# Performance work log

Hardware: AMD Instinct MI355X
Metric: run time of the kernel (lower is better)

Reference implementation:

```python
import jax, jax.numpy as jnp
import numpy as np

B, J, D, W, H, EH, L = 128, 8192, 32, 4, 128, 256, 32
TEMP = 1.0


def _ln(x, g, b, eps=1e-5):
    mu = jnp.mean(x, axis=-1, keepdims=True)
    var = jnp.var(x, axis=-1, keepdims=True)
    return (x - mu) * jax.lax.rsqrt(var + eps) * g + b


def setup_inputs() -> dict:
    key = jax.random.key(0)
    ks = jax.random.split(key, 12)

    def lin(k, fi, fo):
        k1, k2 = jax.random.split(k)
        s = 1.0 / np.sqrt(fi)
        return (jax.random.uniform(k1, (fi, fo), minval=-s, maxval=s, dtype=jnp.float32),
                jax.random.uniform(k2, (fo,), minval=-s, maxval=s, dtype=jnp.float32))

    h_w1, h_b1 = lin(ks[0], 1 + D, H)
    h_w2, h_b2 = lin(ks[1], H, D)
    g_w1, g_b1 = lin(ks[2], D, D // 2)
    g_w2, g_b2 = lin(ks[3], D // 2, W)
    c_w, c_b = lin(ks[4], W * D, D)
    e_w1, e_b1 = lin(ks[5], D, EH)
    e_w2, e_b2 = lin(ks[6], EH, 2 * L)
    return {
        'x': jax.random.normal(ks[7], (B, J), dtype=jnp.float32),
        'mask': jax.random.randint(ks[8], (B, J), 0, 2, dtype=jnp.int32),
        'fe': jax.random.normal(ks[9], (J, D), dtype=jnp.float32),
        'h_w1': h_w1, 'h_b1': h_b1,
        'h_ln1_w': jnp.ones((H,), jnp.float32), 'h_ln1_b': jnp.zeros((H,), jnp.float32),
        'h_w2': h_w2, 'h_b2': h_b2,
        'h_ln2_w': jnp.ones((D,), jnp.float32), 'h_ln2_b': jnp.zeros((D,), jnp.float32),
        'g_w1': g_w1, 'g_b1': g_b1, 'g_w2': g_w2, 'g_b2': g_b2,
        'c_w': c_w, 'c_b': c_b,
        'c_ln_w': jnp.ones((D,), jnp.float32), 'c_ln_b': jnp.zeros((D,), jnp.float32),
        'e_w1': e_w1, 'e_b1': e_b1,
        'e_ln1_w': jnp.ones((EH,), jnp.float32), 'e_ln1_b': jnp.zeros((EH,), jnp.float32),
        'e_w2': e_w2, 'e_b2': e_b2,
        'e_ln2_w': jnp.ones((2 * L,), jnp.float32), 'e_ln2_b': jnp.zeros((2 * L,), jnp.float32),
    }


def _forward(x, mask, fe, h_w1, h_b1, h_ln1_w, h_ln1_b, h_w2, h_b2, h_ln2_w, h_ln2_b,
             g_w1, g_b1, g_w2, g_b2, c_w, c_b, c_ln_w, c_ln_b,
             e_w1, e_b1, e_ln1_w, e_ln1_b, e_w2, e_b2, e_ln2_w, e_ln2_b):
    relu = jax.nn.relu
    # h_in = concat([x, F]) @ h_w1 split into scalar column + shared embedding part
    # (fe @ h_w1[1:]) is [J,H], shared across cells -> avoids materializing [B,J,1+D]
    pre = x[..., None] * h_w1[0][None, None, :] + (fe @ h_w1[1:])[None] + h_b1  # [B,J,H]
    h1 = relu(_ln(pre, h_ln1_w, h_ln1_b))
    h_out = relu(_ln(h1 @ h_w2 + h_b2, h_ln2_w, h_ln2_b))  # [B,J,D]
    raw_gates = relu(h_out @ g_w1 + g_b1) @ g_w2 + g_b2  # [B,J,W]
    logits = jnp.clip(raw_gates * TEMP, -10.0, 10.0)
    logits = jnp.where(mask[..., None] > 0, logits, -1e9)  # masked gather -> -inf fill
    weights = jax.nn.softmax(logits, axis=1)  # softmax over observed junctions
    head_sums = jnp.einsum('bjw,bjd->bwd', weights, h_out)  # [B,W,D]
    comb = relu(_ln(head_sums.reshape(head_sums.shape[0], -1) @ c_w + c_b, c_ln_w, c_ln_b))
    comb = jnp.where((jnp.sum(mask, axis=1) > 0)[:, None], comb, 0.0)  # zero cells -> zeros
    h = relu(_ln(comb @ e_w1 + e_b1, e_ln1_w, e_ln1_b))
    o = relu(_ln(h @ e_w2 + e_b2, e_ln2_w, e_ln2_b))
    mu, logvar = jnp.split(o, 2, axis=-1)
    return mu, logvar


def reference(x, mask, fe, h_w1, h_b1, h_ln1_w, h_ln1_b, h_w2, h_b2, h_ln2_w, h_ln2_b,
              g_w1, g_b1, g_w2, g_b2, c_w, c_b, c_ln_w, c_ln_b,
              e_w1, e_b1, e_ln1_w, e_ln1_b, e_w2, e_b2, e_ln2_w, e_ln2_b):
    return _forward(x, mask, fe, h_w1, h_b1, h_ln1_w, h_ln1_b, h_w2, h_b2, h_ln2_w, h_ln2_b,
                    g_w1, g_b1, g_w2, g_b2, c_w, c_b, c_ln_w, c_ln_b,
                    e_w1, e_b1, e_ln1_w, e_ln1_b, e_w2, e_b2, e_ln2_w, e_ln2_b)
```

## Files before the change

### kernel.cpp

```cpp
#include <hip/hip_runtime.h>
#include <cstdint>

#define BDIM 128
#define JDIM 8192

typedef short s8x __attribute__((ext_vector_type(8)));
typedef float f4x __attribute__((ext_vector_type(4)));
typedef float f2x __attribute__((ext_vector_type(2)));

__device__ __forceinline__ unsigned short bf16u(float f) {
    return __builtin_bit_cast(unsigned short, (__bf16)f);
}
__device__ __forceinline__ unsigned int pkbf(float lo, float hi) {
    return (unsigned int)bf16u(lo) | ((unsigned int)bf16u(hi) << 16);
}
__device__ __forceinline__ f2x upk(unsigned int w) {
    f2x r;
    r.x = __uint_as_float(w << 16);
    r.y = __uint_as_float(w & 0xffff0000u);
    return r;
}
__device__ __forceinline__ f2x pkfma(f2x a, f2x b, f2x c) {
#if __has_builtin(__builtin_elementwise_fma)
    return __builtin_elementwise_fma(a, b, c);
#else
    f2x r; r.x = fmaf(a.x, b.x, c.x); r.y = fmaf(a.y, b.y, c.y); return r;
#endif
}
__device__ __forceinline__ f2x pkmax0(f2x a) {
#if __has_builtin(__builtin_elementwise_max)
    f2x z = {0.f, 0.f};
    return __builtin_elementwise_max(a, z);
#else
    f2x r; r.x = fmaxf(a.x, 0.f); r.y = fmaxf(a.y, 0.f); return r;
#endif
}

template <int CTRL>
__device__ __forceinline__ float dppadd(float x) {
    int y = __builtin_amdgcn_update_dpp(0, __builtin_bit_cast(int, x), CTRL, 0xF, 0xF, true);
    return x + __builtin_bit_cast(float, y);
}
__device__ __forceinline__ float allred16(float x) {
    x = dppadd<0xB1>(x);
    x = dppadd<0x4E>(x);
    x = dppadd<0x141>(x);
    x = dppadd<0x140>(x);
    return x;
}

__global__ __launch_bounds__(128) void k_prep(
    const float* __restrict__ fe, const float* __restrict__ hw1,
    const float* __restrict__ hb1,
    const float* __restrict__ hw2, const float* __restrict__ gw1,
    unsigned short* __restrict__ feWb, float* __restrict__ aux,
    float* __restrict__ scal, uint4* __restrict__ fragW)
{
    const int j = blockIdx.x, h = threadIdx.x;
    float acc = hb1[h];
#pragma unroll
    for (int d = 0; d < 32; ++d)
        acc = fmaf(fe[j * 32 + d], hw1[(1 + d) * 128 + h], acc);
    feWb[(size_t)j * 128 + h] = bf16u(acc);

    const float w0h = hw1[h];
    float s1 = acc, sx = w0h * acc, s2 = acc * acc;
#pragma unroll
    for (int m = 1; m <= 32; m <<= 1) {
        s1 += __shfl_xor(s1, m); sx += __shfl_xor(sx, m); s2 += __shfl_xor(s2, m);
    }
    __shared__ float red[2][3];
    const int wv = threadIdx.x >> 6, ln = threadIdx.x & 63;
    if (ln == 0) { red[wv][0] = s1; red[wv][1] = sx; red[wv][2] = s2; }
    __syncthreads();
    if (threadIdx.x == 0) {
        aux[j * 4 + 0] = (red[0][0] + red[1][0]) * (1.f / 128.f);
        aux[j * 4 + 1] = (red[0][1] + red[1][1]) * (1.f / 128.f);
        aux[j * 4 + 2] = (red[0][2] + red[1][2]) * (1.f / 128.f);
    }
    if (j == 0) {
        float a = w0h, b = w0h * w0h;
#pragma unroll
        for (int m = 1; m <= 32; m <<= 1) { a += __shfl_xor(a, m); b += __shfl_xor(b, m); }
        __syncthreads();
        if (ln == 0) { red[wv][0] = a; red[wv][1] = b; }
        __syncthreads();
        if (threadIdx.x == 0) {
            scal[0] = (red[0][0] + red[1][0]) * (1.f / 128.f);
            scal[1] = (red[0][1] + red[1][1]) * (1.f / 128.f);
        }
        if (threadIdx.x < 64) {
            const int cc = threadIdx.x & 15, gg = threadIdx.x >> 4;
#pragma unroll
            for (int nt = 0; nt < 2; ++nt)
#pragma unroll
                for (int t = 0; t < 4; ++t) {
                    const int kb = 32 * t + 8 * gg, n = 16 * nt + cc;
                    uint4 u;
                    u.x = pkbf(hw2[(kb + 0) * 32 + n], hw2[(kb + 1) * 32 + n]);
                    u.y = pkbf(hw2[(kb + 2) * 32 + n], hw2[(kb + 3) * 32 + n]);
                    u.z = pkbf(hw2[(kb + 4) * 32 + n], hw2[(kb + 5) * 32 + n]);
                    u.w = pkbf(hw2[(kb + 6) * 32 + n], hw2[(kb + 7) * 32 + n]);
                    fragW[(nt * 4 + t) * 64 + threadIdx.x] = u;
                }
            uint4 u;
            u.x = pkbf(gw1[(8 * gg + 0) * 16 + cc], gw1[(8 * gg + 1) * 16 + cc]);
            u.y = pkbf(gw1[(8 * gg + 2) * 16 + cc], gw1[(8 * gg + 3) * 16 + cc]);
            u.z = pkbf(gw1[(8 * gg + 4) * 16 + cc], gw1[(8 * gg + 5) * 16 + cc]);
            u.w = pkbf(gw1[(8 * gg + 6) * 16 + cc], gw1[(8 * gg + 7) * 16 + cc]);
            fragW[8 * 64 + threadIdx.x] = u;
        }
    }
}

__global__ __launch_bounds__(256, 2) void k_main(
    const float* __restrict__ x, const int* __restrict__ mask,
    const unsigned short* __restrict__ feWb, const float* __restrict__ aux,
    const float* __restrict__ scal, const uint4* __restrict__ fragW,
    const float* __restrict__ hw1, const float* __restrict__ ln1w,
    const float* __restrict__ ln1b,
    const float* __restrict__ hb2,
    const float* __restrict__ ln2w, const float* __restrict__ ln2b,
    const float* __restrict__ gb1,
    const float* __restrict__ gw2, const float* __restrict__ gb2,
    float* __restrict__ P, float* __restrict__ SEb, int njb, int jpw)
{
    __shared__ float w0s[128], g1s[128], b1s[128];
    __shared__ float holds[8][576];
    __shared__ float hsL[2048];
    __shared__ float seL[64];

    const int tid = threadIdx.x, l = tid & 63;
    const int wv = __builtin_amdgcn_readfirstlane(tid >> 6);
    const int c = l & 15, g = l >> 4;
    const int bt = blockIdx.y, bx = blockIdx.x;
    const int b0 = bt * 16;

    if (tid < 128) { w0s[tid] = hw1[tid]; g1s[tid] = ln1w[tid]; b1s[tid] = ln1b[tid]; }
    __syncthreads();

    const float mw0 = scal[0], q0 = scal[1];

    s8x wf[2][4];
#pragma unroll
    for (int nt = 0; nt < 2; ++nt)
#pragma unroll
        for (int t = 0; t < 4; ++t)
            wf[nt][t] = __builtin_bit_cast(s8x, fragW[(nt * 4 + t) * 64 + l]);
    const s8x g1f = __builtin_bit_cast(s8x, fragW[8 * 64 + l]);

    const float hb2a = hb2[c],      hb2b = hb2[16 + c];
    const float g2a  = ln2w[c],     g2b  = ln2w[16 + c];
    const float z2a  = ln2b[c],     z2b  = ln2b[16 + c];
    const float gb1c = gb1[c];
    float gw2c[4], gb2v[4];
#pragma unroll
    for (int w = 0; w < 4; ++w) { gw2c[w] = gw2[c * 4 + w]; gb2v[w] = gb2[w]; }

    const int j0 = (bx * 4 + wv) * jpw;
    const float* xrow = x + (size_t)(b0 + c) * JDIM;
    const int*   mrow = mask + (size_t)(b0 + c) * JDIM;

    f2x   hsacc[4][4];
    float seacc[4][4];
#pragma unroll
    for (int r = 0; r < 4; ++r)
#pragma unroll
        for (int w = 0; w < 4; ++w) {
            hsacc[r][w].x = 0.f; hsacc[r][w].y = 0.f; seacc[r][w] = 0.f;
        }

    for (int jj = 0; jj < jpw; ++jj) {
        const int j = j0 + jj;
        const float xv = xrow[j];
        const int   mv = mrow[j];
        const float4 au = *(const float4*)(aux + j * 4);
        const float m1 = au.x, qx = au.y, q2 = au.z;
        const float mu = fmaf(xv, mw0, m1);
        const float e2 = fmaf(xv * xv, q0, fmaf(2.f * xv, qx, q2));
        const float rs = rsqrtf(e2 - mu * mu + 1e-5f);
        const float nms = -mu * rs;
        const f2x xv2 = {xv, xv}, rs2 = {rs, rs}, nm2 = {nms, nms};

        f4x ca = {0.f, 0.f, 0.f, 0.f}, cbv = {0.f, 0.f, 0.f, 0.f};
        const unsigned short* fj = feWb + (size_t)j * 128;
#pragma unroll
        for (int t = 0; t < 4; ++t) {
            const int kb = 32 * t + 8 * g;
            const uint4 fw = *(const uint4*)(fj + kb);
            const unsigned int fwv[4] = {fw.x, fw.y, fw.z, fw.w};
            const f2x* wp = (const f2x*)&w0s[kb];
            const f2x* gp = (const f2x*)&g1s[kb];
            const f2x* bp = (const f2x*)&b1s[kb];
            unsigned int res[4];
#pragma unroll
            for (int p = 0; p < 4; ++p) {
                f2x h2 = pkfma(xv2, wp[p], upk(fwv[p]));
                h2 = pkfma(h2, rs2, nm2);
                h2 = pkfma(h2, gp[p], bp[p]);
                h2 = pkmax0(h2);
                res[p] = pkbf(h2.x, h2.y);
            }
            const uint4 u = make_uint4(res[0], res[1], res[2], res[3]);
            const s8x af = __builtin_bit_cast(s8x, u);
            ca  = __builtin_amdgcn_mfma_f32_16x16x32_bf16(af, wf[0][t], ca,  0, 0, 0);
            cbv = __builtin_amdgcn_mfma_f32_16x16x32_bf16(af, wf[1][t], cbv, 0, 0, 0);
        }

        float v0[4], v1[4], sr[4], qr[4];
#pragma unroll
        for (int r = 0; r < 4; ++r) {
            v0[r] = ca[r] + hb2a;
            v1[r] = cbv[r] + hb2b;
            sr[r] = v0[r] + v1[r];
            qr[r] = v0[r] * v0[r] + v1[r] * v1[r];
        }
#pragma unroll
        for (int r = 0; r < 4; ++r) { sr[r] = allred16(sr[r]); qr[r] = allred16(qr[r]); }
        float ho0[4], ho1[4];
#pragma unroll
        for (int r = 0; r < 4; ++r) {
            const float m2  = sr[r] * 0.03125f;
            const float rs2b = rsqrtf(fmaf(qr[r], 0.03125f, -m2 * m2) + 1e-5f);
            const float nm2b = -m2 * rs2b;
            ho0[r] = fmaxf(fmaf(fmaf(v0[r], rs2b, nm2b), g2a, z2a), 0.f);
            ho1[r] = fmaxf(fmaf(fmaf(v1[r], rs2b, nm2b), g2b, z2b), 0.f);
        }

        float* hp = &holds[wv * 2 + (jj & 1)][0];
#pragma unroll
        for (int r = 0; r < 4; ++r) {
            hp[(4 * g + r) * 36 + c]      = ho0[r];
            hp[(4 * g + r) * 36 + 16 + c] = ho1[r];
        }
        asm volatile("s_waitcnt lgkmcnt(0)" ::: "memory");
        const float4 ra  = *(const float4*)&hp[c * 36 + 8 * g];
        const float4 rb2 = *(const float4*)&hp[c * 36 + 8 * g + 4];
        uint4 ua;
        ua.x = pkbf(ra.x, ra.y);  ua.y = pkbf(ra.z, ra.w);
        ua.z = pkbf(rb2.x, rb2.y); ua.w = pkbf(rb2.z, rb2.w);
        const s8x af2 = __builtin_bit_cast(s8x, ua);
        f4x gc = {0.f, 0.f, 0.f, 0.f};
        gc = __builtin_amdgcn_mfma_f32_16x16x32_bf16(af2, g1f, gc, 0, 0, 0);

        float pw[16];
#pragma unroll
        for (int r = 0; r < 4; ++r) {
            const float g1r = fmaxf(gc[r] + gb1c, 0.f);
#pragma unroll
            for (int w = 0; w < 4; ++w) pw[r * 4 + w] = g1r * gw2c[w];
        }
#pragma unroll
        for (int i = 0; i < 16; ++i) pw[i] = allred16(pw[i]);

        const unsigned bm = (unsigned)__ballot(mv > 0);
        float fm[4];
#pragma unroll
        for (int r = 0; r < 4; ++r) fm[r] = (float)((bm >> (4 * g + r)) & 1u);

#pragma unroll
        for (int r = 0; r < 4; ++r) {
            const f2x ho2 = {ho0[r], ho1[r]};
#pragma unroll
            for (int w = 0; w < 4; ++w) {
                const float lg = __builtin_amdgcn_fmed3f(pw[r * 4 + w] + gb2v[w], -10.f, 10.f);
                const float e  = fm[r] * __builtin_amdgcn_exp2f(
                                     fmaf(lg, 1.44269504089f, -14.4269504089f));
                seacc[r][w] += e;
                const f2x e2v = {e, e};
                hsacc[r][w] = pkfma(e2v, ho2, hsacc[r][w]);
            }
        }
    }

    for (int ww = 0; ww < 4; ++ww) {
        __syncthreads();
        if (wv == ww) {
#pragma unroll
            for (int r = 0; r < 4; ++r)
#pragma unroll
                for (int w = 0; w < 4; ++w)
#pragma unroll
                    for (int nt = 0; nt < 2; ++nt) {
                        const int idx = ((4 * g + r) * 4 + w) * 32 + c + 16 * nt;
                        const float val = nt ? hsacc[r][w].y : hsacc[r][w].x;
                        if (ww == 0) hsL[idx] = val;
                        else         hsL[idx] += val;
                    }
            if (c == 0) {
#pragma unroll
                for (int r = 0; r < 4; ++r)
#pragma unroll
                    for (int w = 0; w < 4; ++w) {
                        const int si = (4 * g + r) * 4 + w;
                        if (ww == 0) seL[si] = seacc[r][w];
                        else         seL[si] += seacc[r][w];
                    }
            }
        }
    }
    __syncthreads();
    const size_t base = ((size_t)bt * njb + bx) * 2048;
    for (int i = tid; i < 2048; i += 256) P[base + i] = hsL[i];
    if (tid < 64) SEb[((size_t)bt * njb + bx) * 64 + tid] = seL[tid];
}

__global__ __launch_bounds__(128) void k_tail(
    const float* __restrict__ P, const float* __restrict__ SEb,
    const float* __restrict__ cw, const float* __restrict__ cbv,
    const float* __restrict__ clnw, const float* __restrict__ clnb,
    const float* __restrict__ ew1, const float* __restrict__ eb1,
    const float* __restrict__ l1w, const float* __restrict__ l1b,
    const float* __restrict__ ew2, const float* __restrict__ eb2,
    const float* __restrict__ l2w, const float* __restrict__ l2b,
    float* __restrict__ out, int njb)
{
    const int b = blockIdx.x, t = threadIdx.x;
    const int bt = b >> 4, bi = b & 15;
    __shared__ float hsLs[128], combL[32], hL[256], seW[4], sred[64], red[4];

    const float* Pb = P + (size_t)bt * njb * 2048 + bi * 128;
    float sacc = 0.f;
#pragma unroll 4
    for (int jc = 0; jc < njb; ++jc) sacc += Pb[(size_t)jc * 2048 + t];

    if (t < 64) {
        const int w = t & 3, part = t >> 2;
        float sp = 0.f;
        for (int q = part; q < njb; q += 16)
            sp += SEb[((size_t)bt * njb + q) * 64 + bi * 4 + w];
        sred[t] = sp;
    }
    __syncthreads();
    if (t < 4) {
        float v = 0.f;
#pragma unroll
        for (int sl = 0; sl < 16; ++sl) v += sred[sl * 4 + t];
        seW[t] = v;
    }
    __syncthreads();
    const bool has = seW[0] > 0.f;
    hsLs[t] = has ? sacc / seW[t >> 5] : 0.f;
    __syncthreads();

    if (t < 32) {
        float cv = cbv[t];
#pragma unroll 4
        for (int f = 0; f < 128; ++f) cv = fmaf(hsLs[f], cw[f * 32 + t], cv);
        float s = cv, q = cv * cv;
#pragma unroll
        for (int m = 1; m <= 16; m <<= 1) { s += __shfl_xor(s, m); q += __shfl_xor(q, m); }
        const float mu = s * (1.f / 32.f);
        const float rsg = rsqrtf(fmaf(q, 1.f / 32.f, -mu * mu) + 1e-5f);
        const float v = fmaf(fmaf(cv, rsg, -mu * rsg), clnw[t], clnb[t]);
        combL[t] = has ? fmaxf(v, 0.f) : 0.f;
    }
    __syncthreads();

    float h0 = eb1[t], h1v = eb1[t + 128];
#pragma unroll 4
    for (int d = 0; d < 32; ++d) {
        const float cd = combL[d];
        h0  = fmaf(cd, ew1[d * 256 + t], h0);
        h1v = fmaf(cd, ew1[d * 256 + t + 128], h1v);
    }
    {
        float s = h0 + h1v, q = h0 * h0 + h1v * h1v;
#pragma unroll
        for (int m = 1; m <= 32; m <<= 1) { s += __shfl_xor(s, m); q += __shfl_xor(q, m); }
        const int wv = t >> 6, ln = t & 63;
        if (ln == 0) { red[wv * 2] = s; red[wv * 2 + 1] = q; }
    }
    __syncthreads();
    {
        const float S = red[0] + red[2], Q = red[1] + red[3];
        const float mu1 = S * (1.f / 256.f);
        const float rs1 = rsqrtf(fmaf(Q, 1.f / 256.f, -mu1 * mu1) + 1e-5f);
        hL[t]       = fmaxf(fmaf(fmaf(h0,  rs1, -mu1 * rs1), l1w[t],       l1b[t]),       0.f);
        hL[t + 128] = fmaxf(fmaf(fmaf(h1v, rs1, -mu1 * rs1), l1w[t + 128], l1b[t + 128]), 0.f);
    }
    __syncthreads();

    if (t < 64) {
        float ov = eb2[t];
#pragma unroll 4
        for (int m = 0; m < 256; ++m) ov = fmaf(hL[m], ew2[m * 64 + t], ov);
        float s = ov, q = ov * ov;
#pragma unroll
        for (int m = 1; m <= 32; m <<= 1) { s += __shfl_xor(s, m); q += __shfl_xor(q, m); }
        const float mu2 = s * (1.f / 64.f);
        const float rs2 = rsqrtf(fmaf(q, 1.f / 64.f, -mu2 * mu2) + 1e-5f);
        const float o = fmaxf(fmaf(fmaf(ov, rs2, -mu2 * rs2), l2w[t], l2b[t]), 0.f);
        if (t < 32) out[b * 32 + t] = o;
        else        out[4096 + b * 32 + (t - 32)] = o;
    }
}

extern "C" void kernel_launch(void* const* d_in, const int* in_sizes, int n_in,
                              void* d_out, int out_size, void* d_ws, size_t ws_size,
                              hipStream_t stream)
{
    (void)in_sizes; (void)n_in; (void)out_size;
    const float* x    = (const float*)d_in[0];
    const int*   mask = (const int*)d_in[1];
    const float* fe   = (const float*)d_in[2];
    const float* hw1  = (const float*)d_in[3];
    const float* hb1  = (const float*)d_in[4];
    const float* ln1w = (const float*)d_in[5];
    const float* ln1b = (const float*)d_in[6];
    const float* hw2  = (const float*)d_in[7];
    const float* hb2  = (const float*)d_in[8];
    const float* ln2w = (const float*)d_in[9];
    const float* ln2b = (const float*)d_in[10];
    const float* gw1  = (const float*)d_in[11];
    const float* gb1  = (const float*)d_in[12];
    const float* gw2  = (const float*)d_in[13];
    const float* gb2  = (const float*)d_in[14];
    const float* cw   = (const float*)d_in[15];
    const float* cbv  = (const float*)d_in[16];
    const float* clnw = (const float*)d_in[17];
    const float* clnb = (const float*)d_in[18];
    const float* ew1  = (const float*)d_in[19];
    const float* eb1  = (const float*)d_in[20];
    const float* l1w  = (const float*)d_in[21];
    const float* l1b  = (const float*)d_in[22];
    const float* ew2  = (const float*)d_in[23];
    const float* eb2  = (const float*)d_in[24];
    const float* l2w  = (const float*)d_in[25];
    const float* l2b  = (const float*)d_in[26];

    const size_t fragOff = (2u << 20) + (128u << 10) + 256u;
    const size_t base    = fragOff + 9u * 64u * 16u;
    int NJB = 128;
    {
        const size_t need = base + (size_t)8 * 128 * 2048 * 4 + (size_t)8 * 128 * 64 * 4;
        if (ws_size < need) NJB = 64;
    }
    const int JPW = JDIM / (NJB * 4);

    char* ws = (char*)d_ws;
    unsigned short* feWb = (unsigned short*)ws;
    float* aux   = (float*)(ws + (2u << 20));
    float* scal  = (float*)(ws + (2u << 20) + (128u << 10));
    uint4* fragW = (uint4*)(ws + fragOff);
    float* P     = (float*)(ws + base);
    float* SEb   = (float*)(ws + base + (size_t)8 * NJB * 2048 * 4);

    hipLaunchKernelGGL(k_prep, dim3(JDIM), dim3(128), 0, stream,
                       fe, hw1, hb1, hw2, gw1, feWb, aux, scal, fragW);
    hipLaunchKernelGGL(k_main, dim3(NJB, 8), dim3(256), 0, stream,
                       x, mask, feWb, aux, scal, fragW,
                       hw1, ln1w, ln1b, hb2, ln2w, ln2b,
                       gb1, gw2, gb2, P, SEb, NJB, JPW);
    hipLaunchKernelGGL(k_tail, dim3(BDIM), dim3(128), 0, stream,
                       P, SEb, cw, cbv, clnw, clnb,
                       ew1, eb1, l1w, l1b, ew2, eb2, l2w, l2b,
                       (float*)d_out, NJB);
}
```

Measured before the change: 247.4 us.

## Process junction pairs per iteration, template JPW, batch prep rows, fuse DPP adds

The main loop now handles two junctions per iteration, so the MFMA chains, LDS round-trips and DPP reductions of two independent rows can interleave. JPW becomes a template parameter so the loop bound is known at compile time. The prep kernel processes eight junctions per block and keeps the hw1 column in registers, replacing 8192 tiny blocks with 1024. The all-reduce now uses inline-asm DPP-fused v_add, and the clamp/exp2 constants are folded into a single fma plus med3. Register pressure rises with the doubled live state, which may limit occupancy under the launch bound of two blocks per SIMD.

```diff
diff --git a/kernel.cpp b/kernel.cpp
--- a/kernel.cpp
+++ b/kernel.cpp
@@ -21,31 +21,23 @@
     return r;
 }
 __device__ __forceinline__ f2x pkfma(f2x a, f2x b, f2x c) {
-#if __has_builtin(__builtin_elementwise_fma)
     return __builtin_elementwise_fma(a, b, c);
-#else
-    f2x r; r.x = fmaf(a.x, b.x, c.x); r.y = fmaf(a.y, b.y, c.y); return r;
-#endif
 }
 __device__ __forceinline__ f2x pkmax0(f2x a) {
-#if __has_builtin(__builtin_elementwise_max)
     f2x z = {0.f, 0.f};
     return __builtin_elementwise_max(a, z);
-#else
-    f2x r; r.x = fmaxf(a.x, 0.f); r.y = fmaxf(a.y, 0.f); return r;
-#endif
-}
-
-template <int CTRL>
-__device__ __forceinline__ float dppadd(float x) {
-    int y = __builtin_amdgcn_update_dpp(0, __builtin_bit_cast(int, x), CTRL, 0xF, 0xF, true);
-    return x + __builtin_bit_cast(float, y);
-}
+}
+
 __device__ __forceinline__ float allred16(float x) {
-    x = dppadd<0xB1>(x);
-    x = dppadd<0x4E>(x);
-    x = dppadd<0x141>(x);
-    x = dppadd<0x140>(x);
+    float t;
+    asm("v_add_f32 %0, %1, %1 quad_perm:[1,0,3,2] row_mask:0xf bank_mask:0xf"
+        : "=v"(t) : "v"(x));
+    asm("v_add_f32 %0, %1, %1 quad_perm:[2,3,0,1] row_mask:0xf bank_mask:0xf"
+        : "=v"(x) : "v"(t));
+    asm("v_add_f32 %0, %1, %1 row_half_mirror row_mask:0xf bank_mask:0xf"
+        : "=v"(t) : "v"(x));
+    asm("v_add_f32 %0, %1, %1 row_mirror row_mask:0xf bank_mask:0xf"
+        : "=v"(x) : "v"(t));
     return x;
 }
 
@@ -56,41 +48,50 @@
     unsigned short* __restrict__ feWb, float* __restrict__ aux,
     float* __restrict__ scal, uint4* __restrict__ fragW)
 {
-    const int j = blockIdx.x, h = threadIdx.x;
-    float acc = hb1[h];
-#pragma unroll
-    for (int d = 0; d < 32; ++d)
-        acc = fmaf(fe[j * 32 + d], hw1[(1 + d) * 128 + h], acc);
-    feWb[(size_t)j * 128 + h] = bf16u(acc);
-
+    const int h = threadIdx.x;
+    __shared__ float red[2][3];
+    const int wv = h >> 6, ln = h & 63;
+    float w1r[32];
+#pragma unroll
+    for (int d = 0; d < 32; ++d) w1r[d] = hw1[(1 + d) * 128 + h];
+    const float hb = hb1[h];
     const float w0h = hw1[h];
-    float s1 = acc, sx = w0h * acc, s2 = acc * acc;
-#pragma unroll
-    for (int m = 1; m <= 32; m <<= 1) {
-        s1 += __shfl_xor(s1, m); sx += __shfl_xor(sx, m); s2 += __shfl_xor(s2, m);
-    }
-    __shared__ float red[2][3];
-    const int wv = threadIdx.x >> 6, ln = threadIdx.x & 63;
-    if (ln == 0) { red[wv][0] = s1; red[wv][1] = sx; red[wv][2] = s2; }
-    __syncthreads();
-    if (threadIdx.x == 0) {
-        aux[j * 4 + 0] = (red[0][0] + red[1][0]) * (1.f / 128.f);
-        aux[j * 4 + 1] = (red[0][1] + red[1][1]) * (1.f / 128.f);
-        aux[j * 4 + 2] = (red[0][2] + red[1][2]) * (1.f / 128.f);
-    }
-    if (j == 0) {
+
+    for (int q = 0; q < 8; ++q) {
+        const int j = blockIdx.x * 8 + q;
+        float acc = hb;
+#pragma unroll
+        for (int d = 0; d < 32; ++d) acc = fmaf(fe[j * 32 + d], w1r[d], acc);
+        feWb[(size_t)j * 128 + h] = bf16u(acc);
+
+        float s1 = acc, sx = w0h * acc, s2 = acc * acc;
+#pragma unroll
+        for (int m = 1; m <= 32; m <<= 1) {
+            s1 += __shfl_xor(s1, m); sx += __shfl_xor(sx, m); s2 += __shfl_xor(s2, m);
+        }
+        if (q) __syncthreads();
+        if (ln == 0) { red[wv][0] = s1; red[wv][1] = sx; red[wv][2] = s2; }
+        __syncthreads();
+        if (h == 0) {
+            aux[j * 4 + 0] = (red[0][0] + red[1][0]) * (1.f / 128.f);
+            aux[j * 4 + 1] = (red[0][1] + red[1][1]) * (1.f / 128.f);
+            aux[j * 4 + 2] = (red[0][2] + red[1][2]) * (1.f / 128.f);
+        }
+    }
+
+    if (blockIdx.x == 0) {
         float a = w0h, b = w0h * w0h;
 #pragma unroll
         for (int m = 1; m <= 32; m <<= 1) { a += __shfl_xor(a, m); b += __shfl_xor(b, m); }
         __syncthreads();
         if (ln == 0) { red[wv][0] = a; red[wv][1] = b; }
         __syncthreads();
-        if (threadIdx.x == 0) {
+        if (h == 0) {
             scal[0] = (red[0][0] + red[1][0]) * (1.f / 128.f);
             scal[1] = (red[0][1] + red[1][1]) * (1.f / 128.f);
         }
-        if (threadIdx.x < 64) {
-            const int cc = threadIdx.x & 15, gg = threadIdx.x >> 4;
+        if (h < 64) {
+            const int cc = h & 15, gg = h >> 4;
 #pragma unroll
             for (int nt = 0; nt < 2; ++nt)
 #pragma unroll
@@ -101,18 +102,19 @@
                     u.y = pkbf(hw2[(kb + 2) * 32 + n], hw2[(kb + 3) * 32 + n]);
                     u.z = pkbf(hw2[(kb + 4) * 32 + n], hw2[(kb + 5) * 32 + n]);
                     u.w = pkbf(hw2[(kb + 6) * 32 + n], hw2[(kb + 7) * 32 + n]);
-                    fragW[(nt * 4 + t) * 64 + threadIdx.x] = u;
+                    fragW[(nt * 4 + t) * 64 + h] = u;
                 }
             uint4 u;
             u.x = pkbf(gw1[(8 * gg + 0) * 16 + cc], gw1[(8 * gg + 1) * 16 + cc]);
             u.y = pkbf(gw1[(8 * gg + 2) * 16 + cc], gw1[(8 * gg + 3) * 16 + cc]);
             u.z = pkbf(gw1[(8 * gg + 4) * 16 + cc], gw1[(8 * gg + 5) * 16 + cc]);
             u.w = pkbf(gw1[(8 * gg + 6) * 16 + cc], gw1[(8 * gg + 7) * 16 + cc]);
-            fragW[8 * 64 + threadIdx.x] = u;
-        }
-    }
-}
-
+            fragW[8 * 64 + h] = u;
+        }
+    }
+}
+
+template <int JPW>
 __global__ __launch_bounds__(256, 2) void k_main(
     const float* __restrict__ x, const int* __restrict__ mask,
     const unsigned short* __restrict__ feWb, const float* __restrict__ aux,
@@ -123,7 +125,7 @@
     const float* __restrict__ ln2w, const float* __restrict__ ln2b,
     const float* __restrict__ gb1,
     const float* __restrict__ gw2, const float* __restrict__ gb2,
-    float* __restrict__ P, float* __restrict__ SEb, int njb, int jpw)
+    float* __restrict__ P, float* __restrict__ SEb, int njb)
 {
     __shared__ float w0s[128], g1s[128], b1s[128];
     __shared__ float holds[8][576];
@@ -153,11 +155,15 @@
     const float g2a  = ln2w[c],     g2b  = ln2w[16 + c];
     const float z2a  = ln2b[c],     z2b  = ln2b[16 + c];
     const float gb1c = gb1[c];
-    float gw2c[4], gb2v[4];
-#pragma unroll
-    for (int w = 0; w < 4; ++w) { gw2c[w] = gw2[c * 4 + w]; gb2v[w] = gb2[w]; }
-
-    const int j0 = (bx * 4 + wv) * jpw;
+    const float L2E  = 1.442695040888963f;
+    float gw2c[4], gb2l[4];
+#pragma unroll
+    for (int w = 0; w < 4; ++w) {
+        gw2c[w] = gw2[c * 4 + w];
+        gb2l[w] = fmaf(gb2[w], L2E, -10.f * L2E);
+    }
+
+    const int j0 = (bx * 4 + wv) * JPW;
     const float* xrow = x + (size_t)(b0 + c) * JDIM;
     const int*   mrow = mask + (size_t)(b0 + c) * JDIM;
 
@@ -170,105 +176,128 @@
             hsacc[r][w].x = 0.f; hsacc[r][w].y = 0.f; seacc[r][w] = 0.f;
         }
 
-    for (int jj = 0; jj < jpw; ++jj) {
-        const int j = j0 + jj;
-        const float xv = xrow[j];
-        const int   mv = mrow[j];
-        const float4 au = *(const float4*)(aux + j * 4);
-        const float m1 = au.x, qx = au.y, q2 = au.z;
-        const float mu = fmaf(xv, mw0, m1);
-        const float e2 = fmaf(xv * xv, q0, fmaf(2.f * xv, qx, q2));
-        const float rs = rsqrtf(e2 - mu * mu + 1e-5f);
-        const float nms = -mu * rs;
-        const f2x xv2 = {xv, xv}, rs2 = {rs, rs}, nm2 = {nms, nms};
-
-        f4x ca = {0.f, 0.f, 0.f, 0.f}, cbv = {0.f, 0.f, 0.f, 0.f};
-        const unsigned short* fj = feWb + (size_t)j * 128;
-#pragma unroll
-        for (int t = 0; t < 4; ++t) {
-            const int kb = 32 * t + 8 * g;
-            const uint4 fw = *(const uint4*)(fj + kb);
-            const unsigned int fwv[4] = {fw.x, fw.y, fw.z, fw.w};
-            const f2x* wp = (const f2x*)&w0s[kb];
-            const f2x* gp = (const f2x*)&g1s[kb];
-            const f2x* bp = (const f2x*)&b1s[kb];
-            unsigned int res[4];
-#pragma unroll
-            for (int p = 0; p < 4; ++p) {
-                f2x h2 = pkfma(xv2, wp[p], upk(fwv[p]));
-                h2 = pkfma(h2, rs2, nm2);
-                h2 = pkfma(h2, gp[p], bp[p]);
-                h2 = pkmax0(h2);
-                res[p] = pkbf(h2.x, h2.y);
-            }
-            const uint4 u = make_uint4(res[0], res[1], res[2], res[3]);
-            const s8x af = __builtin_bit_cast(s8x, u);
-            ca  = __builtin_amdgcn_mfma_f32_16x16x32_bf16(af, wf[0][t], ca,  0, 0, 0);
-            cbv = __builtin_amdgcn_mfma_f32_16x16x32_bf16(af, wf[1][t], cbv, 0, 0, 0);
-        }
-
-        float v0[4], v1[4], sr[4], qr[4];
-#pragma unroll
-        for (int r = 0; r < 4; ++r) {
-            v0[r] = ca[r] + hb2a;
-            v1[r] = cbv[r] + hb2b;
-            sr[r] = v0[r] + v1[r];
-            qr[r] = v0[r] * v0[r] + v1[r] * v1[r];
-        }
-#pragma unroll
-        for (int r = 0; r < 4; ++r) { sr[r] = allred16(sr[r]); qr[r] = allred16(qr[r]); }
-        float ho0[4], ho1[4];
-#pragma unroll
-        for (int r = 0; r < 4; ++r) {
-            const float m2  = sr[r] * 0.03125f;
-            const float rs2b = rsqrtf(fmaf(qr[r], 0.03125f, -m2 * m2) + 1e-5f);
-            const float nm2b = -m2 * rs2b;
-            ho0[r] = fmaxf(fmaf(fmaf(v0[r], rs2b, nm2b), g2a, z2a), 0.f);
-            ho1[r] = fmaxf(fmaf(fmaf(v1[r], rs2b, nm2b), g2b, z2b), 0.f);
-        }
-
-        float* hp = &holds[wv * 2 + (jj & 1)][0];
-#pragma unroll
-        for (int r = 0; r < 4; ++r) {
-            hp[(4 * g + r) * 36 + c]      = ho0[r];
-            hp[(4 * g + r) * 36 + 16 + c] = ho1[r];
+    for (int jp = 0; jp < JPW / 2; ++jp) {
+        const int jb = j0 + jp * 2;
+
+        float xv[2], rsv[2], nms[2]; int mv[2];
+#pragma unroll
+        for (int p = 0; p < 2; ++p) {
+            xv[p] = xrow[jb + p];
+            mv[p] = mrow[jb + p];
+            const float4 au = *(const float4*)(aux + (size_t)(jb + p) * 4);
+            const float mu = fmaf(xv[p], mw0, au.x);
+            const float e2 = fmaf(xv[p] * xv[p], q0, fmaf(2.f * xv[p], au.y, au.z));
+            rsv[p] = rsqrtf(e2 - mu * mu + 1e-5f);
+            nms[p] = -mu * rsv[p];
+        }
+
+        f4x ca[2], cb[2];
+#pragma unroll
+        for (int p = 0; p < 2; ++p) { ca[p] = f4x{0.f,0.f,0.f,0.f}; cb[p] = f4x{0.f,0.f,0.f,0.f}; }
+#pragma unroll
+        for (int p = 0; p < 2; ++p) {
+            const f2x xv2 = {xv[p], xv[p]}, rs2 = {rsv[p], rsv[p]}, nm2 = {nms[p], nms[p]};
+            const unsigned short* fj = feWb + (size_t)(jb + p) * 128;
+#pragma unroll
+            for (int t = 0; t < 4; ++t) {
+                const int kb = 32 * t + 8 * g;
+                const uint4 fw = *(const uint4*)(fj + kb);
+                const unsigned int fwv[4] = {fw.x, fw.y, fw.z, fw.w};
+                const f2x* wp = (const f2x*)&w0s[kb];
+                const f2x* gp = (const f2x*)&g1s[kb];
+                const f2x* bp = (const f2x*)&b1s[kb];
+                unsigned int res[4];
+#pragma unroll
+                for (int q = 0; q < 4; ++q) {
+                    f2x h2 = pkfma(xv2, wp[q], upk(fwv[q]));
+                    h2 = pkfma(h2, rs2, nm2);
+                    h2 = pkfma(h2, gp[q], bp[q]);
+                    h2 = pkmax0(h2);
+                    res[q] = pkbf(h2.x, h2.y);
+                }
+                const uint4 u = make_uint4(res[0], res[1], res[2], res[3]);
+                const s8x af = __builtin_bit_cast(s8x, u);
+                ca[p] = __builtin_amdgcn_mfma_f32_16x16x32_bf16(af, wf[0][t], ca[p], 0, 0, 0);
+                cb[p] = __builtin_amdgcn_mfma_f32_16x16x32_bf16(af, wf[1][t], cb[p], 0, 0, 0);
+            }
+        }
+
+        float ho0[2][4], ho1[2][4];
+#pragma unroll
+        for (int p = 0; p < 2; ++p) {
+            float v0[4], v1[4], sr[4], qr[4];
+#pragma unroll
+            for (int r = 0; r < 4; ++r) {
+                v0[r] = ca[p][r] + hb2a;
+                v1[r] = cb[p][r] + hb2b;
+                sr[r] = v0[r] + v1[r];
+                qr[r] = v0[r] * v0[r] + v1[r] * v1[r];
+            }
+#pragma unroll
+            for (int r = 0; r < 4; ++r) { sr[r] = allred16(sr[r]); qr[r] = allred16(qr[r]); }
+#pragma unroll
+            for (int r = 0; r < 4; ++r) {
+                const float m2   = sr[r] * 0.03125f;
+                const float rs2b = rsqrtf(fmaf(qr[r], 0.03125f, -m2 * m2) + 1e-5f);
+                const float nm2b = -m2 * rs2b;
+                ho0[p][r] = fmaxf(fmaf(fmaf(v0[r], rs2b, nm2b), g2a, z2a), 0.f);
+                ho1[p][r] = fmaxf(fmaf(fmaf(v1[r], rs2b, nm2b), g2b, z2b), 0.f);
+            }
+        }
+
+#pragma unroll
+        for (int p = 0; p < 2; ++p) {
+            float* hp = &holds[wv * 2 + p][0];
+#pragma unroll
+            for (int r = 0; r < 4; ++r) {
+                hp[(4 * g + r) * 36 + c]      = ho0[p][r];
+                hp[(4 * g + r) * 36 + 16 + c] = ho1[p][r];
+            }
         }
         asm volatile("s_waitcnt lgkmcnt(0)" ::: "memory");
-        const float4 ra  = *(const float4*)&hp[c * 36 + 8 * g];
-        const float4 rb2 = *(const float4*)&hp[c * 36 + 8 * g + 4];
-        uint4 ua;
-        ua.x = pkbf(ra.x, ra.y);  ua.y = pkbf(ra.z, ra.w);
-        ua.z = pkbf(rb2.x, rb2.y); ua.w = pkbf(rb2.z, rb2.w);
-        const s8x af2 = __builtin_bit_cast(s8x, ua);
-        f4x gc = {0.f, 0.f, 0.f, 0.f};
-        gc = __builtin_amdgcn_mfma_f32_16x16x32_bf16(af2, g1f, gc, 0, 0, 0);
-
-        float pw[16];
-#pragma unroll
-        for (int r = 0; r < 4; ++r) {
-            const float g1r = fmaxf(gc[r] + gb1c, 0.f);
-#pragma unroll
-            for (int w = 0; w < 4; ++w) pw[r * 4 + w] = g1r * gw2c[w];
-        }
-#pragma unroll
-        for (int i = 0; i < 16; ++i) pw[i] = allred16(pw[i]);
-
-        const unsigned bm = (unsigned)__ballot(mv > 0);
-        float fm[4];
-#pragma unroll
-        for (int r = 0; r < 4; ++r) fm[r] = (float)((bm >> (4 * g + r)) & 1u);
-
-#pragma unroll
-        for (int r = 0; r < 4; ++r) {
-            const f2x ho2 = {ho0[r], ho1[r]};
-#pragma unroll
-            for (int w = 0; w < 4; ++w) {
-                const float lg = __builtin_amdgcn_fmed3f(pw[r * 4 + w] + gb2v[w], -10.f, 10.f);
-                const float e  = fm[r] * __builtin_amdgcn_exp2f(
-                                     fmaf(lg, 1.44269504089f, -14.4269504089f));
-                seacc[r][w] += e;
-                const f2x e2v = {e, e};
-                hsacc[r][w] = pkfma(e2v, ho2, hsacc[r][w]);
+        f4x gc[2];
+#pragma unroll
+        for (int p = 0; p < 2; ++p) {
+            const float* hp = &holds[wv * 2 + p][0];
+            const float4 ra  = *(const float4*)&hp[c * 36 + 8 * g];
+            const float4 rb2 = *(const float4*)&hp[c * 36 + 8 * g + 4];
+            uint4 ua;
+            ua.x = pkbf(ra.x, ra.y);   ua.y = pkbf(ra.z, ra.w);
+            ua.z = pkbf(rb2.x, rb2.y); ua.w = pkbf(rb2.z, rb2.w);
+            const s8x af2 = __builtin_bit_cast(s8x, ua);
+            f4x z = {0.f, 0.f, 0.f, 0.f};
+            gc[p] = __builtin_amdgcn_mfma_f32_16x16x32_bf16(af2, g1f, z, 0, 0, 0);
+        }
+
+#pragma unroll
+        for (int p = 0; p < 2; ++p) {
+            float pw[16];
+#pragma unroll
+            for (int r = 0; r < 4; ++r) {
+                const float g1r = fmaxf(gc[p][r] + gb1c, 0.f);
+#pragma unroll
+                for (int w = 0; w < 4; ++w) pw[r * 4 + w] = g1r * gw2c[w];
+            }
+#pragma unroll
+            for (int i = 0; i < 16; ++i) pw[i] = allred16(pw[i]);
+
+            const unsigned bm = (unsigned)__ballot(mv[p] > 0);
+            float fm[4];
+#pragma unroll
+            for (int r = 0; r < 4; ++r) fm[r] = (float)((bm >> (4 * g + r)) & 1u);
+
+#pragma unroll
+            for (int r = 0; r < 4; ++r) {
+                const f2x ho2 = {ho0[p][r], ho1[p][r]};
+#pragma unroll
+                for (int w = 0; w < 4; ++w) {
+                    float t = fmaf(pw[r * 4 + w], L2E, gb2l[w]);
+                    t = __builtin_amdgcn_fmed3f(t, -20.f * L2E, 0.f);
+                    const float e = fm[r] * __builtin_amdgcn_exp2f(t);
+                    seacc[r][w] += e;
+                    const f2x e2v = {e, e};
+                    hsacc[r][w] = pkfma(e2v, ho2, hsacc[r][w]);
+                }
             }
         }
     }
@@ -436,7 +465,6 @@
         const size_t need = base + (size_t)8 * 128 * 2048 * 4 + (size_t)8 * 128 * 64 * 4;
         if (ws_size < need) NJB = 64;
     }
-    const int JPW = JDIM / (NJB * 4);
 
     char* ws = (char*)d_ws;
     unsigned short* feWb = (unsigned short*)ws;
@@ -446,12 +474,18 @@
     float* P     = (float*)(ws + base);
     float* SEb   = (float*)(ws + base + (size_t)8 * NJB * 2048 * 4);
 
-    hipLaunchKernelGGL(k_prep, dim3(JDIM), dim3(128), 0, stream,
+    hipLaunchKernelGGL(k_prep, dim3(JDIM / 8), dim3(128), 0, stream,
                        fe, hw1, hb1, hw2, gw1, feWb, aux, scal, fragW);
-    hipLaunchKernelGGL(k_main, dim3(NJB, 8), dim3(256), 0, stream,
-                       x, mask, feWb, aux, scal, fragW,
-                       hw1, ln1w, ln1b, hb2, ln2w, ln2b,
-                       gb1, gw2, gb2, P, SEb, NJB, JPW);
+    if (NJB == 128)
+        hipLaunchKernelGGL((k_main<16>), dim3(128, 8), dim3(256), 0, stream,
+                           x, mask, feWb, aux, scal, fragW,
+                           hw1, ln1w, ln1b, hb2, ln2w, ln2b,
+                           gb1, gw2, gb2, P, SEb, 128);
+    else
+        hipLaunchKernelGGL((k_main<32>), dim3(64, 8), dim3(256), 0, stream,
+                           x, mask, feWb, aux, scal, fragW,
+                           hw1, ln1w, ln1b, hb2, ln2w, ln2b,
+                           gb1, gw2, gb2, P, SEb, 64);
     hipLaunchKernelGGL(k_tail, dim3(BDIM), dim3(128), 0, stream,
                        P, SEb, cw, cbv, clnw, clnb,
                        ew1, eb1, l1w, l1b, ew2, eb2, l2w, l2b,
```

Result: faster. 237.3 us (-4.1%).
